# Kernel optimization log

Measured on AMD Instinct MI355X. Metric: run time of the kernel, lower is better.

Reference implementation:

```python
import jax, jax.numpy as jnp
import numpy as np

N_NODES = 100_000
N_EDGES = 1_600_000
IN_DIM = 128
HIDDEN = 128
OUT_DIM = 64
N_LAYERS = 8
ALPHA = 0.1  # GCN2Conv alpha; beta = 1.0 since theta/layer not given


def setup_inputs() -> dict:
    key = jax.random.key(0)
    ks = jax.random.split(key, 6)
    x = jax.random.normal(ks[0], (N_NODES, IN_DIM), dtype=jnp.float32)
    edge_index = jax.random.randint(ks[1], (2, N_EDGES), 0, N_NODES, dtype=jnp.int64)
    W_in = jax.random.normal(ks[2], (IN_DIM, HIDDEN), dtype=jnp.float32) / np.sqrt(IN_DIM)
    b_in = jnp.zeros((HIDDEN,), jnp.float32)
    conv_w = jax.random.normal(ks[3], (N_LAYERS, HIDDEN, HIDDEN), dtype=jnp.float32) / np.sqrt(HIDDEN)
    W_out = jax.random.normal(ks[4], (HIDDEN, OUT_DIM), dtype=jnp.float32) / np.sqrt(HIDDEN)
    b_out = jnp.zeros((OUT_DIM,), jnp.float32)
    return {"x": x, "edge_index": edge_index, "W_in": W_in, "b_in": b_in,
            "conv_w": conv_w, "W_out": W_out, "b_out": b_out}


def reference(x, edge_index, W_in, b_in, conv_w, W_out, b_out):
    N = x.shape[0]
    # gcn_norm with self-loops: A_hat = D^-1/2 (A + I) D^-1/2
    loops = jnp.arange(N, dtype=edge_index.dtype)
    ei = jnp.concatenate([edge_index, jnp.stack([loops, loops])], axis=1)
    row, col = ei[0], ei[1]  # source, target
    deg = jax.ops.segment_sum(jnp.ones(ei.shape[1], x.dtype), col, num_segments=N)
    dinv = jnp.where(deg > 0, jax.lax.rsqrt(deg), 0.0)
    norm = dinv[row] * dinv[col]  # [E+N]

    h = jax.nn.relu(x @ W_in + b_in)  # input projection
    x0 = h  # initial residual
    for l in range(conv_w.shape[0]):
        # sparse neighbor aggregation: out[i] = sum_{(j->i)} norm * h[j]
        agg = jax.ops.segment_sum(h[row] * norm[:, None], col, num_segments=N)
        support = (1.0 - ALPHA) * agg + ALPHA * x0  # initial residual mix
        h = jax.nn.relu(support @ conv_w[l])  # beta=1 -> out = support @ W
        # dropout: identity in eval mode
    return h @ W_out + b_out
```

## Files before the change

kernel.cpp:

```cpp
#include <hip/hip_runtime.h>
#include <hip/hip_fp16.h>
#include <cstdint>
#include <cstddef>


#define HID 128

using f16x8 = __attribute__((ext_vector_type(8))) _Float16;
using f16x4 = __attribute__((ext_vector_type(4))) _Float16;
using f32x4 = __attribute__((ext_vector_type(4))) float;


__global__ void k_hist(const int* __restrict__ col, int E, int* __restrict__ cnt) {
  int e = blockIdx.x * blockDim.x + threadIdx.x;
  if (e < E) atomicAdd(&cnt[col[e]], 1);
}

__global__ __launch_bounds__(256) void k_blocksum_dinv(const int* __restrict__ cnt,
                                                       int* __restrict__ bsum,
                                                       float* __restrict__ dinv, int N) {
  __shared__ int s[256];
  int t = threadIdx.x;
  int i = blockIdx.x * 256 + t;
  int v = (i < N) ? cnt[i] : 0;
  if (i < N) dinv[i] = rsqrtf((float)v + 1.0f);
  s[t] = v;
  __syncthreads();
  for (int off = 128; off > 0; off >>= 1) {
    if (t < off) s[t] += s[t + off];
    __syncthreads();
  }
  if (t == 0) bsum[blockIdx.x] = s[0];
}

__global__ __launch_bounds__(512) void k_scan_bsum(const int* __restrict__ bsum,
                                                   int* __restrict__ bofs, int nb) {
  __shared__ int s[512];
  __shared__ int carry;
  int t = threadIdx.x;
  if (t == 0) carry = 0;
  __syncthreads();
  for (int base = 0; base < nb; base += 512) {
    int i = base + t;
    int v = (i < nb) ? bsum[i] : 0;
    s[t] = v;
    __syncthreads();
    for (int off = 1; off < 512; off <<= 1) {
      int a = (t >= off) ? s[t - off] : 0;
      __syncthreads();
      s[t] += a;
      __syncthreads();
    }
    if (i < nb) bofs[i] = carry + s[t] - v;
    __syncthreads();
    if (t == 0) carry += s[511];
    __syncthreads();
  }
}

__global__ __launch_bounds__(256) void k_scan_write(const int* __restrict__ cnt,
                                                    const int* __restrict__ bofs,
                                                    int* __restrict__ row_ptr, int N) {
  __shared__ int s[256];
  int t = threadIdx.x;
  int i = blockIdx.x * 256 + t;
  int v = (i < N) ? cnt[i] : 0;
  s[t] = v;
  __syncthreads();
  for (int off = 1; off < 256; off <<= 1) {
    int a = (t >= off) ? s[t - off] : 0;
    __syncthreads();
    s[t] += a;
    __syncthreads();
  }
  int excl = bofs[blockIdx.x] + s[t] - v;
  if (i < N) row_ptr[i] = excl;
  if (i == N - 1) row_ptr[N] = excl + v;
}

__global__ void k_fill(const int* __restrict__ row, const int* __restrict__ col, int E,
                       const int* __restrict__ row_ptr, int* __restrict__ cnt,
                       int* __restrict__ csr_src) {
  int e = blockIdx.x * blockDim.x + threadIdx.x;
  if (e >= E) return;
  int r = row[e], c = col[e];
  int p = row_ptr[c] + atomicSub(&cnt[c], 1) - 1;
  csr_src[p] = r;
}

__global__ void k_wprep(const float* __restrict__ Wc, const float* __restrict__ W_in,
                        const float* __restrict__ W_out, _Float16* __restrict__ Wt,
                        int L) {
  int id = blockIdx.x * blockDim.x + threadIdx.x;
  int nl = L * 16384;
  if (id < nl) {
    int l = id >> 14, r = id & 16383;
    int k = r >> 7, n = r & 127;
    Wt[(size_t)l * 16384 + n * 128 + k] = (_Float16)Wc[(size_t)l * 16384 + k * 128 + n];
  } else if (id < nl + 16384) {
    int r = id - nl;
    int k = r >> 7, n = r & 127;
    Wt[(size_t)nl + n * 128 + k] = (_Float16)W_in[k * 128 + n];
  } else if (id < nl + 16384 + 8192) {
    int r = id - nl - 16384;
    int k = r >> 6, n = r & 63;
    Wt[(size_t)(nl + 16384) + n * 128 + k] = (_Float16)W_out[k * 64 + n];
  }
}


__global__ __launch_bounds__(256) void k_aggregate16(
    const _Float16* __restrict__ h, const _Float16* __restrict__ x0h,
    const float* __restrict__ dinv, const int* __restrict__ row_ptr,
    const int* __restrict__ csr_src, _Float16* __restrict__ support, int N) {
  int node = blockIdx.x * 8 + (threadIdx.x >> 5);
  if (node >= N) return;
  int lane = threadIdx.x & 31;
  int d0 = lane * 4;
  int beg = row_ptr[node], end = row_ptr[node + 1];
  float di = dinv[node];

  f16x4 v0 = *(const f16x4*)(h + (size_t)node * HID + d0);
  f16x4 xv = *(const f16x4*)(x0h + (size_t)node * HID + d0);

  float a0 = di * (float)v0[0], a1 = di * (float)v0[1];
  float a2 = di * (float)v0[2], a3 = di * (float)v0[3];

  int j = beg;
  for (; j + 8 <= end; j += 8) {
    int s0 = csr_src[j],     s1 = csr_src[j + 1], s2 = csr_src[j + 2], s3 = csr_src[j + 3];
    int s4 = csr_src[j + 4], s5 = csr_src[j + 5], s6 = csr_src[j + 6], s7 = csr_src[j + 7];
    f16x4 r0 = *(const f16x4*)(h + (size_t)s0 * HID + d0);
    f16x4 r1 = *(const f16x4*)(h + (size_t)s1 * HID + d0);
    f16x4 r2 = *(const f16x4*)(h + (size_t)s2 * HID + d0);
    f16x4 r3 = *(const f16x4*)(h + (size_t)s3 * HID + d0);
    f16x4 r4 = *(const f16x4*)(h + (size_t)s4 * HID + d0);
    f16x4 r5 = *(const f16x4*)(h + (size_t)s5 * HID + d0);
    f16x4 r6 = *(const f16x4*)(h + (size_t)s6 * HID + d0);
    f16x4 r7 = *(const f16x4*)(h + (size_t)s7 * HID + d0);
    float w0 = dinv[s0], w1 = dinv[s1], w2 = dinv[s2], w3 = dinv[s3];
    float w4 = dinv[s4], w5 = dinv[s5], w6 = dinv[s6], w7 = dinv[s7];
    a0 = fmaf(w0, (float)r0[0], a0); a1 = fmaf(w0, (float)r0[1], a1);
    a2 = fmaf(w0, (float)r0[2], a2); a3 = fmaf(w0, (float)r0[3], a3);
    a0 = fmaf(w1, (float)r1[0], a0); a1 = fmaf(w1, (float)r1[1], a1);
    a2 = fmaf(w1, (float)r1[2], a2); a3 = fmaf(w1, (float)r1[3], a3);
    a0 = fmaf(w2, (float)r2[0], a0); a1 = fmaf(w2, (float)r2[1], a1);
    a2 = fmaf(w2, (float)r2[2], a2); a3 = fmaf(w2, (float)r2[3], a3);
    a0 = fmaf(w3, (float)r3[0], a0); a1 = fmaf(w3, (float)r3[1], a1);
    a2 = fmaf(w3, (float)r3[2], a2); a3 = fmaf(w3, (float)r3[3], a3);
    a0 = fmaf(w4, (float)r4[0], a0); a1 = fmaf(w4, (float)r4[1], a1);
    a2 = fmaf(w4, (float)r4[2], a2); a3 = fmaf(w4, (float)r4[3], a3);
    a0 = fmaf(w5, (float)r5[0], a0); a1 = fmaf(w5, (float)r5[1], a1);
    a2 = fmaf(w5, (float)r5[2], a2); a3 = fmaf(w5, (float)r5[3], a3);
    a0 = fmaf(w6, (float)r6[0], a0); a1 = fmaf(w6, (float)r6[1], a1);
    a2 = fmaf(w6, (float)r6[2], a2); a3 = fmaf(w6, (float)r6[3], a3);
    a0 = fmaf(w7, (float)r7[0], a0); a1 = fmaf(w7, (float)r7[1], a1);
    a2 = fmaf(w7, (float)r7[2], a2); a3 = fmaf(w7, (float)r7[3], a3);
  }
  if (j + 4 <= end) {
    int s0 = csr_src[j], s1 = csr_src[j + 1], s2 = csr_src[j + 2], s3 = csr_src[j + 3];
    f16x4 r0 = *(const f16x4*)(h + (size_t)s0 * HID + d0);
    f16x4 r1 = *(const f16x4*)(h + (size_t)s1 * HID + d0);
    f16x4 r2 = *(const f16x4*)(h + (size_t)s2 * HID + d0);
    f16x4 r3 = *(const f16x4*)(h + (size_t)s3 * HID + d0);
    float w0 = dinv[s0], w1 = dinv[s1], w2 = dinv[s2], w3 = dinv[s3];
    a0 = fmaf(w0, (float)r0[0], a0); a1 = fmaf(w0, (float)r0[1], a1);
    a2 = fmaf(w0, (float)r0[2], a2); a3 = fmaf(w0, (float)r0[3], a3);
    a0 = fmaf(w1, (float)r1[0], a0); a1 = fmaf(w1, (float)r1[1], a1);
    a2 = fmaf(w1, (float)r1[2], a2); a3 = fmaf(w1, (float)r1[3], a3);
    a0 = fmaf(w2, (float)r2[0], a0); a1 = fmaf(w2, (float)r2[1], a1);
    a2 = fmaf(w2, (float)r2[2], a2); a3 = fmaf(w2, (float)r2[3], a3);
    a0 = fmaf(w3, (float)r3[0], a0); a1 = fmaf(w3, (float)r3[1], a1);
    a2 = fmaf(w3, (float)r3[2], a2); a3 = fmaf(w3, (float)r3[3], a3);
    j += 4;
  }
  for (; j < end; ++j) {
    int s = csr_src[j];
    float w = dinv[s];
    f16x4 r = *(const f16x4*)(h + (size_t)s * HID + d0);
    a0 = fmaf(w, (float)r[0], a0); a1 = fmaf(w, (float)r[1], a1);
    a2 = fmaf(w, (float)r[2], a2); a3 = fmaf(w, (float)r[3], a3);
  }
  float s9 = 0.9f * di;
  f16x4 o;
  o[0] = (_Float16)(s9 * a0 + 0.1f * (float)xv[0]);
  o[1] = (_Float16)(s9 * a1 + 0.1f * (float)xv[1]);
  o[2] = (_Float16)(s9 * a2 + 0.1f * (float)xv[2]);
  o[3] = (_Float16)(s9 * a3 + 0.1f * (float)xv[3]);
  *(f16x4*)(support + (size_t)node * HID + d0) = o;
}


template <int NC, bool RELU, bool BIAS, bool AF32, bool OHALF>
__global__ __launch_bounds__(256) void k_mfma_gemm(const void* __restrict__ Av,
                                                   const _Float16* __restrict__ Bt,
                                                   const float* __restrict__ bias,
                                                   void* __restrict__ Cv, int M) {
  constexpr int NT = NC / 16;
  int tid = threadIdx.x;
  int w = tid >> 6, l = tid & 63;
  int lm = l & 15, kg = l >> 4;
  int row0 = blockIdx.x * 128 + w * 32;
  int r0 = min(row0 + lm, M - 1);
  int r1 = min(row0 + 16 + lm, M - 1);

  f32x4 acc[2][NT];
#pragma unroll
  for (int mt = 0; mt < 2; ++mt)
#pragma unroll
    for (int nt = 0; nt < NT; ++nt) acc[mt][nt] = (f32x4){0.f, 0.f, 0.f, 0.f};

#pragma unroll
  for (int ks = 0; ks < 128; ks += 32) {
    f16x8 a0, a1;
    if (AF32) {
      const float* Af = (const float*)Av;
      float4 p0 = *(const float4*)(Af + (size_t)r0 * 128 + ks + kg * 8);
      float4 p1 = *(const float4*)(Af + (size_t)r0 * 128 + ks + kg * 8 + 4);
      float4 q0 = *(const float4*)(Af + (size_t)r1 * 128 + ks + kg * 8);
      float4 q1 = *(const float4*)(Af + (size_t)r1 * 128 + ks + kg * 8 + 4);
      a0[0] = (_Float16)p0.x; a0[1] = (_Float16)p0.y; a0[2] = (_Float16)p0.z; a0[3] = (_Float16)p0.w;
      a0[4] = (_Float16)p1.x; a0[5] = (_Float16)p1.y; a0[6] = (_Float16)p1.z; a0[7] = (_Float16)p1.w;
      a1[0] = (_Float16)q0.x; a1[1] = (_Float16)q0.y; a1[2] = (_Float16)q0.z; a1[3] = (_Float16)q0.w;
      a1[4] = (_Float16)q1.x; a1[5] = (_Float16)q1.y; a1[6] = (_Float16)q1.z; a1[7] = (_Float16)q1.w;
    } else {
      const _Float16* Ah = (const _Float16*)Av;
      a0 = *(const f16x8*)(Ah + (size_t)r0 * 128 + ks + kg * 8);
      a1 = *(const f16x8*)(Ah + (size_t)r1 * 128 + ks + kg * 8);
    }
#pragma unroll
    for (int nt = 0; nt < NT; ++nt) {
      f16x8 b = *(const f16x8*)(Bt + (size_t)(nt * 16 + lm) * 128 + ks + kg * 8);
      acc[0][nt] = __builtin_amdgcn_mfma_f32_16x16x32_f16(a0, b, acc[0][nt], 0, 0, 0);
      acc[1][nt] = __builtin_amdgcn_mfma_f32_16x16x32_f16(a1, b, acc[1][nt], 0, 0, 0);
    }
  }

#pragma unroll
  for (int mt = 0; mt < 2; ++mt) {
#pragma unroll
    for (int nt = 0; nt < NT; ++nt) {
      int colc = nt * 16 + lm;
      float bv = BIAS ? bias[colc] : 0.0f;
#pragma unroll
      for (int i = 0; i < 4; ++i) {
        int r = row0 + mt * 16 + kg * 4 + i;
        if (r >= M) continue;
        float v = acc[mt][nt][i] + bv;
        if (RELU) v = fmaxf(v, 0.0f);
        if (OHALF)
          ((_Float16*)Cv)[(size_t)r * NC + colc] = (_Float16)v;
        else
          ((float*)Cv)[(size_t)r * NC + colc] = v;
      }
    }
  }
}


extern "C" void kernel_launch(void* const* d_in, const int* in_sizes, int n_in,
                              void* d_out, int out_size, void* d_ws, size_t ws_size,
                              hipStream_t stream) {
  const float* x     = (const float*)d_in[0];
  const int*   ei    = (const int*)d_in[1];
  const float* W_in  = (const float*)d_in[2];
  const float* b_in  = (const float*)d_in[3];
  const float* Wc    = (const float*)d_in[4];
  const float* W_out = (const float*)d_in[5];
  const float* b_out = (const float*)d_in[6];
  float* out = (float*)d_out;

  const int N = in_sizes[0] / HID;
  const int E = in_sizes[1] / 2;
  const int L = in_sizes[4] / (HID * HID);
  const int nb = (N + 255) / 256;
  const int* row = ei;
  const int* col = ei + E;

  char* p = (char*)d_ws;
  auto alloc = [&](size_t bytes) {
    char* q = p;
    p += (bytes + 255) & ~(size_t)255;
    return q;
  };
  _Float16* x0h   = (_Float16*)alloc((size_t)N * HID * 2);
  _Float16* sup16 = (_Float16*)alloc((size_t)N * HID * 2);
  _Float16* h16   = (_Float16*)alloc((size_t)N * HID * 2);
  _Float16* Wt    = (_Float16*)alloc((size_t)(L * 16384 + 16384 + 8192) * 2);
  int*    cnt     = (int*)alloc((size_t)N * 4);
  int*    row_ptr = (int*)alloc((size_t)(N + 1) * 4);
  int*    bsum    = (int*)alloc((size_t)nb * 4);
  int*    bofs    = (int*)alloc((size_t)nb * 4);
  float*  dinv    = (float*)alloc((size_t)N * 4);
  int*    csr_src = (int*)alloc((size_t)E * 4);
  (void)ws_size; (void)n_in; (void)out_size;

  const _Float16* Wt_in  = Wt + (size_t)L * 16384;
  const _Float16* Wt_out = Wt + (size_t)L * 16384 + 16384;

  hipMemsetAsync(cnt, 0, (size_t)N * 4, stream);

  int nw = L * 16384 + 16384 + 8192;
  k_wprep<<<(nw + 255) / 256, 256, 0, stream>>>(Wc, W_in, W_out, Wt, L);
  k_hist<<<(E + 255) / 256, 256, 0, stream>>>(col, E, cnt);
  k_blocksum_dinv<<<nb, 256, 0, stream>>>(cnt, bsum, dinv, N);
  k_scan_bsum<<<1, 512, 0, stream>>>(bsum, bofs, nb);
  k_scan_write<<<nb, 256, 0, stream>>>(cnt, bofs, row_ptr, N);
  k_fill<<<(E + 255) / 256, 256, 0, stream>>>(row, col, E, row_ptr, cnt, csr_src);

  int ggrid = (N + 127) / 128;
  k_mfma_gemm<128, true, true, true, true><<<ggrid, 256, 0, stream>>>(x, Wt_in, b_in,
                                                                      x0h, N);

  const _Float16* hin = x0h;
  int agrid = (N + 7) / 8;
  for (int l = 0; l < L; ++l) {
    k_aggregate16<<<agrid, 256, 0, stream>>>(hin, x0h, dinv, row_ptr, csr_src,
                                             sup16, N);
    k_mfma_gemm<128, true, false, false, true><<<ggrid, 256, 0, stream>>>(
        sup16, Wt + (size_t)l * 16384, nullptr, h16, N);
    hin = h16;
  }
  k_mfma_gemm<64, false, true, false, false><<<ggrid, 256, 0, stream>>>(hin, Wt_out,
                                                                        b_out, out, N);
}
```

Measured before the change: 990.2 us.

## Build CSR with two-pass bucketed radix partition instead of global atomics

Replaces the per-node histogram, multi-kernel scan and atomic scatter fill with a two-level partition: edges are first bucketed by the target's high bits (512-node buckets) using LDS histograms, then each bucket is sorted locally in shared memory to produce row_ptr, dinv and csr_src. This aims to cut global atomic contention and random scattered writes during CSR construction. It adds an extra temp buffer and pass over edges, and it depends on N being small enough for at most 256 buckets, spilling to direct global writes when a bucket exceeds the LDS slice capacity.

```diff
diff --git a/kernel.cpp b/kernel.cpp
--- a/kernel.cpp
+++ b/kernel.cpp
@@ -5,66 +5,37 @@
 
 
 #define HID 128
+#define BKSH 9
+#define RMAX 256
+#define SLICE_CAP 11264
 
 using f16x8 = __attribute__((ext_vector_type(8))) _Float16;
 using f16x4 = __attribute__((ext_vector_type(4))) _Float16;
 using f32x4 = __attribute__((ext_vector_type(4))) float;
 
 
-__global__ void k_hist(const int* __restrict__ col, int E, int* __restrict__ cnt) {
-  int e = blockIdx.x * blockDim.x + threadIdx.x;
-  if (e < E) atomicAdd(&cnt[col[e]], 1);
-}
-
-__global__ __launch_bounds__(256) void k_blocksum_dinv(const int* __restrict__ cnt,
-                                                       int* __restrict__ bsum,
-                                                       float* __restrict__ dinv, int N) {
+__global__ __launch_bounds__(512) void k_bhist(const int* __restrict__ col, int E,
+                                               int* __restrict__ bcnt, int R) {
+  __shared__ int lh[RMAX];
+  int tid = threadIdx.x;
+  if (tid < R) lh[tid] = 0;
+  __syncthreads();
+  int base = blockIdx.x * 4096;
+#pragma unroll
+  for (int i = 0; i < 8; ++i) {
+    int e = base + i * 512 + tid;
+    if (e < E) atomicAdd(&lh[col[e] >> BKSH], 1);
+  }
+  __syncthreads();
+  if (tid < R && lh[tid]) atomicAdd(&bcnt[tid], lh[tid]);
+}
+
+__global__ __launch_bounds__(256) void k_scan196(const int* __restrict__ bcnt,
+                                                 int* __restrict__ gb,
+                                                 int* __restrict__ gfront, int R) {
   __shared__ int s[256];
   int t = threadIdx.x;
-  int i = blockIdx.x * 256 + t;
-  int v = (i < N) ? cnt[i] : 0;
-  if (i < N) dinv[i] = rsqrtf((float)v + 1.0f);
-  s[t] = v;
-  __syncthreads();
-  for (int off = 128; off > 0; off >>= 1) {
-    if (t < off) s[t] += s[t + off];
-    __syncthreads();
-  }
-  if (t == 0) bsum[blockIdx.x] = s[0];
-}
-
-__global__ __launch_bounds__(512) void k_scan_bsum(const int* __restrict__ bsum,
-                                                   int* __restrict__ bofs, int nb) {
-  __shared__ int s[512];
-  __shared__ int carry;
-  int t = threadIdx.x;
-  if (t == 0) carry = 0;
-  __syncthreads();
-  for (int base = 0; base < nb; base += 512) {
-    int i = base + t;
-    int v = (i < nb) ? bsum[i] : 0;
-    s[t] = v;
-    __syncthreads();
-    for (int off = 1; off < 512; off <<= 1) {
-      int a = (t >= off) ? s[t - off] : 0;
-      __syncthreads();
-      s[t] += a;
-      __syncthreads();
-    }
-    if (i < nb) bofs[i] = carry + s[t] - v;
-    __syncthreads();
-    if (t == 0) carry += s[511];
-    __syncthreads();
-  }
-}
-
-__global__ __launch_bounds__(256) void k_scan_write(const int* __restrict__ cnt,
-                                                    const int* __restrict__ bofs,
-                                                    int* __restrict__ row_ptr, int N) {
-  __shared__ int s[256];
-  int t = threadIdx.x;
-  int i = blockIdx.x * 256 + t;
-  int v = (i < N) ? cnt[i] : 0;
+  int v = (t < R) ? bcnt[t] : 0;
   s[t] = v;
   __syncthreads();
   for (int off = 1; off < 256; off <<= 1) {
@@ -73,19 +44,94 @@
     s[t] += a;
     __syncthreads();
   }
-  int excl = bofs[blockIdx.x] + s[t] - v;
-  if (i < N) row_ptr[i] = excl;
-  if (i == N - 1) row_ptr[N] = excl + v;
-}
-
-__global__ void k_fill(const int* __restrict__ row, const int* __restrict__ col, int E,
-                       const int* __restrict__ row_ptr, int* __restrict__ cnt,
-                       int* __restrict__ csr_src) {
-  int e = blockIdx.x * blockDim.x + threadIdx.x;
-  if (e >= E) return;
-  int r = row[e], c = col[e];
-  int p = row_ptr[c] + atomicSub(&cnt[c], 1) - 1;
-  csr_src[p] = r;
+  int excl = s[t] - v;
+  if (t < R) {
+    gb[t] = excl;
+    gfront[t] = excl;
+  }
+  if (t == 255) gb[R] = s[255];
+}
+
+__global__ __launch_bounds__(512) void k_partA(const int* __restrict__ row,
+                                               const int* __restrict__ col, int E,
+                                               int* __restrict__ gfront,
+                                               int* __restrict__ tmp, int R) {
+  __shared__ int lh[RMAX], base[RMAX], fr[RMAX];
+  int tid = threadIdx.x;
+  if (tid < R) { lh[tid] = 0; fr[tid] = 0; }
+  __syncthreads();
+  int b0 = blockIdx.x * 4096;
+  int r[8], c[8], bk[8];
+  bool ok[8];
+#pragma unroll
+  for (int i = 0; i < 8; ++i) {
+    int e = b0 + i * 512 + tid;
+    ok[i] = e < E;
+    if (ok[i]) {
+      r[i] = row[e];
+      c[i] = col[e];
+      bk[i] = c[i] >> BKSH;
+      atomicAdd(&lh[bk[i]], 1);
+    }
+  }
+  __syncthreads();
+  if (tid < R && lh[tid] > 0) base[tid] = atomicAdd(&gfront[tid], lh[tid]);
+  __syncthreads();
+#pragma unroll
+  for (int i = 0; i < 8; ++i) {
+    if (ok[i]) {
+      int o = atomicAdd(&fr[bk[i]], 1);
+      tmp[base[bk[i]] + o] = (r[i] << BKSH) | (c[i] & ((1 << BKSH) - 1));
+    }
+  }
+}
+
+__global__ __launch_bounds__(512) void k_partB(const int* __restrict__ tmp,
+                                               const int* __restrict__ gb,
+                                               int* __restrict__ csr_src,
+                                               int* __restrict__ row_ptr,
+                                               float* __restrict__ dinv, int N, int E,
+                                               int R) {
+  __shared__ int h2[512], pref[512];
+  __shared__ int slice[SLICE_CAP];
+  int tid = threadIdx.x;
+  int b = blockIdx.x;
+  int lo = gb[b], hi = gb[b + 1];
+  int cnt = hi - lo;
+  h2[tid] = 0;
+  __syncthreads();
+  for (int k = tid; k < cnt; k += 512) atomicAdd(&h2[tmp[lo + k] & 511], 1);
+  __syncthreads();
+  int v = h2[tid];
+  pref[tid] = v;
+  __syncthreads();
+  for (int off = 1; off < 512; off <<= 1) {
+    int a = (tid >= off) ? pref[tid - off] : 0;
+    __syncthreads();
+    pref[tid] += a;
+    __syncthreads();
+  }
+  int excl = pref[tid] - v;
+  int node = b * 512 + tid;
+  if (node < N) {
+    row_ptr[node] = lo + excl;
+    dinv[node] = rsqrtf((float)v + 1.0f);
+  }
+  if (b == R - 1 && tid == 0) row_ptr[N] = E;
+  __syncthreads();
+  pref[tid] = excl;
+  h2[tid] = 0;
+  __syncthreads();
+  for (int k = tid; k < cnt; k += 512) {
+    int ent = tmp[lo + k];
+    int nd = ent & 511;
+    int o = pref[nd] + atomicAdd(&h2[nd], 1);
+    if (o < SLICE_CAP) slice[o] = ent >> BKSH;
+    else csr_src[lo + o] = ent >> BKSH;
+  }
+  __syncthreads();
+  int lim = cnt < SLICE_CAP ? cnt : SLICE_CAP;
+  for (int k = tid; k < lim; k += 512) csr_src[lo + k] = slice[k];
 }
 
 __global__ void k_wprep(const float* __restrict__ Wc, const float* __restrict__ W_in,
@@ -273,7 +319,7 @@
   const int N = in_sizes[0] / HID;
   const int E = in_sizes[1] / 2;
   const int L = in_sizes[4] / (HID * HID);
-  const int nb = (N + 255) / 256;
+  const int R = (N + 511) >> BKSH;
   const int* row = ei;
   const int* col = ei + E;
 
@@ -287,26 +333,27 @@
   _Float16* sup16 = (_Float16*)alloc((size_t)N * HID * 2);
   _Float16* h16   = (_Float16*)alloc((size_t)N * HID * 2);
   _Float16* Wt    = (_Float16*)alloc((size_t)(L * 16384 + 16384 + 8192) * 2);
-  int*    cnt     = (int*)alloc((size_t)N * 4);
   int*    row_ptr = (int*)alloc((size_t)(N + 1) * 4);
-  int*    bsum    = (int*)alloc((size_t)nb * 4);
-  int*    bofs    = (int*)alloc((size_t)nb * 4);
   float*  dinv    = (float*)alloc((size_t)N * 4);
   int*    csr_src = (int*)alloc((size_t)E * 4);
+  int*    tmp     = (int*)alloc((size_t)E * 4);
+  int*    bcnt    = (int*)alloc((size_t)R * 4);
+  int*    gb      = (int*)alloc((size_t)(R + 1) * 4);
+  int*    gfront  = (int*)alloc((size_t)R * 4);
   (void)ws_size; (void)n_in; (void)out_size;
 
   const _Float16* Wt_in  = Wt + (size_t)L * 16384;
   const _Float16* Wt_out = Wt + (size_t)L * 16384 + 16384;
 
-  hipMemsetAsync(cnt, 0, (size_t)N * 4, stream);
+  hipMemsetAsync(bcnt, 0, (size_t)R * 4, stream);
 
   int nw = L * 16384 + 16384 + 8192;
+  int nbe = (E + 4095) / 4096;
   k_wprep<<<(nw + 255) / 256, 256, 0, stream>>>(Wc, W_in, W_out, Wt, L);
-  k_hist<<<(E + 255) / 256, 256, 0, stream>>>(col, E, cnt);
-  k_blocksum_dinv<<<nb, 256, 0, stream>>>(cnt, bsum, dinv, N);
-  k_scan_bsum<<<1, 512, 0, stream>>>(bsum, bofs, nb);
-  k_scan_write<<<nb, 256, 0, stream>>>(cnt, bofs, row_ptr, N);
-  k_fill<<<(E + 255) / 256, 256, 0, stream>>>(row, col, E, row_ptr, cnt, csr_src);
+  k_bhist<<<nbe, 512, 0, stream>>>(col, E, bcnt, R);
+  k_scan196<<<1, 256, 0, stream>>>(bcnt, gb, gfront, R);
+  k_partA<<<nbe, 512, 0, stream>>>(row, col, E, gfront, tmp, R);
+  k_partB<<<R, 512, 0, stream>>>(tmp, gb, csr_src, row_ptr, dinv, N, E, R);
 
   int ggrid = (N + 127) / 128;
   k_mfma_gemm<128, true, true, true, true><<<ggrid, 256, 0, stream>>>(x, Wt_in, b_in,
```

Result: faster. 856.5 us (-13.5%).
